# Performance work log

Hardware: AMD Instinct MI355X
Metric: run time of the kernel (lower is better)

## Reference

```python
import jax, jax.numpy as jnp
import numpy as np

N_NODES = 75000
N_EDGES = 1200000


def gcn_conv(x, src, dst, W, b, n):
    # linear transform first (PyG GCNConv applies lin before propagate)
    h = x @ W  # [n, out]
    # add self loops
    loop = jnp.arange(n, dtype=src.dtype)
    s = jnp.concatenate([src, loop])
    d = jnp.concatenate([dst, loop])
    # symmetric normalization: deg computed on destination after self-loops
    deg = jnp.zeros((n,), dtype=h.dtype).at[d].add(1.0)
    dinv = jnp.where(deg > 0, jax.lax.rsqrt(deg), 0.0)
    norm = dinv[s] * dinv[d]  # [E+n]
    msgs = h[s] * norm[:, None]  # gather + scale, [E+n, out]
    out = jax.ops.segment_sum(msgs, d, num_segments=n)  # scatter-add
    return out + b


def setup_inputs() -> dict:
    key = jax.random.key(0)
    ks = jax.random.split(key, 6)
    x = jax.random.normal(ks[0], (N_NODES, 64), dtype=jnp.float32)
    edge_index = jax.random.randint(ks[1], (2, N_EDGES), 0, N_NODES, dtype=jnp.int64)
    # Glorot-ish scaled weights
    W1 = jax.random.normal(ks[2], (64, 64), dtype=jnp.float32) * (1.0 / np.sqrt(64))
    b1 = jax.random.normal(ks[3], (64,), dtype=jnp.float32) * 0.01
    W2 = jax.random.normal(ks[4], (64, 16), dtype=jnp.float32) * (1.0 / np.sqrt(64))
    b2 = jax.random.normal(ks[5], (16,), dtype=jnp.float32) * 0.01
    return {"x": x, "edge_index": edge_index, "W1": W1, "b1": b1, "W2": W2, "b2": b2}


def reference(x, edge_index, W1, b1, W2, b2):
    src, dst = edge_index[0], edge_index[1]
    h = gcn_conv(x, src, dst, W1, b1, N_NODES)
    h = jax.nn.relu(h)
    # dropout is identity in eval mode
    out = gcn_conv(h, src, dst, W2, b2, N_NODES)
    return out
```

## Files before the change

kernel.cpp:

```cpp
#include <hip/hip_runtime.h>


#define NBSHIFT 9
#define BUCKET_NODES 512
#define CAP 10240
#define CHA 8192
#define TA 512
#define TB 512
#define MAXNB 160

__device__ __forceinline__ unsigned bfpack(float a, float b) {
  unsigned ua = __float_as_uint(a), ub = __float_as_uint(b);
  ua += 0x7fffu + ((ua >> 16) & 1u);
  ub += 0x7fffu + ((ub >> 16) & 1u);
  return (ua >> 16) | (ub & 0xffff0000u);
}

__launch_bounds__(TA)
__global__ void kA_bucket(const int* __restrict__ src, const int* __restrict__ dst,
                          int* __restrict__ bucketCur, int* __restrict__ bucketArr,
                          int NB, int E) {
  __shared__ int stage[CHA];
  __shared__ unsigned char binOf[CHA];
  __shared__ int cnt[MAXNB];
  __shared__ int off[MAXNB];
  __shared__ int gpos[MAXNB];
  __shared__ int cursor[MAXNB];
  __shared__ int scanbuf[256];
  int t = threadIdx.x;
  int e0 = blockIdx.x * CHA;

  for (int i = t; i < NB; i += TA) cnt[i] = 0;
  __syncthreads();
  for (int i = t; i < CHA; i += TA) {
    int e = e0 + i;
    if (e < E) atomicAdd(&cnt[dst[e] >> NBSHIFT], 1);
  }
  __syncthreads();
  if (t < 256) scanbuf[t] = (t < NB) ? cnt[t] : 0;
  __syncthreads();
  for (int o = 1; o < 256; o <<= 1) {
    int add = (t < 256 && t >= o) ? scanbuf[t - o] : 0;
    __syncthreads();
    if (t < 256) scanbuf[t] += add;
    __syncthreads();
  }
  if (t < NB) {
    off[t] = scanbuf[t] - cnt[t];
    cursor[t] = off[t];
    gpos[t] = (cnt[t] > 0) ? atomicAdd(&bucketCur[t], cnt[t]) : 0;
  }
  __syncthreads();
  for (int i = t; i < CHA; i += TA) {
    int e = e0 + i;
    if (e < E) {
      int d = dst[e], s = src[e];
      int b = d >> NBSHIFT;
      int p = atomicAdd(&cursor[b], 1);
      stage[p] = (s << NBSHIFT) | (d & (BUCKET_NODES - 1));
      binOf[p] = (unsigned char)b;
    }
  }
  __syncthreads();
  int total = scanbuf[255];
  for (int i = t; i < total; i += TA) {
    int b = binOf[i];
    int destIdx = gpos[b] + (i - off[b]);
    if (destIdx < CAP) bucketArr[b * CAP + destIdx] = stage[i];
  }
}

__global__ void kB_scan(const int* __restrict__ bucketCur, int* __restrict__ bucketBase,
                        int* __restrict__ rp, int NB, int N) {
  __shared__ int s[256];
  int t = threadIdx.x;
  int v = (t < NB) ? min(bucketCur[t], CAP) : 0;
  s[t] = v;
  __syncthreads();
  for (int o = 1; o < 256; o <<= 1) {
    int add = (t >= o) ? s[t - o] : 0;
    __syncthreads();
    s[t] += add;
    __syncthreads();
  }
  if (t < NB) bucketBase[t] = s[t] - v;
  if (t == NB - 1) {
    bucketBase[NB] = s[t];
    rp[N] = s[t];
  }
}

__launch_bounds__(TB)
__global__ void kB_fill(const int* __restrict__ bucketArr, const int* __restrict__ bucketCur,
                        const int* __restrict__ bucketBase,
                        int* __restrict__ rp, float* __restrict__ dinv,
                        int* __restrict__ col, int N) {
  __shared__ int hist[BUCKET_NODES];
  __shared__ int noff[BUCKET_NODES];
  __shared__ int cur[BUCKET_NODES];
  __shared__ int colStage[CAP];
  int b = blockIdx.x;
  int t = threadIdx.x;
  int nE = min(bucketCur[b], CAP);
  int base = b * CAP;

  hist[t] = 0;
  __syncthreads();
  for (int i = t; i < nE; i += TB) {
    atomicAdd(&hist[bucketArr[base + i] & (BUCKET_NODES - 1)], 1);
  }
  __syncthreads();
  int myv = hist[t];
  noff[t] = myv;
  __syncthreads();
  for (int o = 1; o < BUCKET_NODES; o <<= 1) {
    int add = (t >= o) ? noff[t - o] : 0;
    __syncthreads();
    noff[t] += add;
    __syncthreads();
  }
  int excl = noff[t] - myv;
  cur[t] = excl;
  int gnode = b * BUCKET_NODES + t;
  if (gnode < N) {
    rp[gnode] = bucketBase[b] + excl;
    dinv[gnode] = rsqrtf((float)(myv + 1));
  }
  __syncthreads();
  for (int i = t; i < nE; i += TB) {
    int v = bucketArr[base + i];
    int p = atomicAdd(&cur[v & (BUCKET_NODES - 1)], 1);
    colStage[p] = v >> NBSHIFT;
  }
  __syncthreads();
  int gb = bucketBase[b];
  for (int i = t; i < nE; i += TB) col[gb + i] = colStage[i];
}

__launch_bounds__(256)
__global__ void k_gemm64(const float4* __restrict__ X4, const float4* __restrict__ W4,
                         const float* __restrict__ dinv, uint2* __restrict__ outb,
                         int n) {
  __shared__ float4 Xs[64 * 17];
  __shared__ float4 Ws[64 * 16];
  int t = threadIdx.x;
  int base = blockIdx.x * 64;
  {
    int rr = t >> 2, q = t & 3;
    int r = base + rr;
    #pragma unroll
    for (int c = 0; c < 4; c++) {
      float4 v = make_float4(0.f, 0.f, 0.f, 0.f);
      if (r < n) v = X4[r * 16 + q * 4 + c];
      Xs[rr * 17 + q * 4 + c] = v;
      Ws[t + 256 * c] = W4[t + 256 * c];
    }
  }
  __syncthreads();

  int tx = t & 15, ty = t >> 4;
  float4 a0 = make_float4(0.f, 0.f, 0.f, 0.f), a1 = a0, a2 = a0, a3 = a0;
  #pragma unroll
  for (int kb = 0; kb < 16; kb++) {
    float4 x0 = Xs[(ty * 4 + 0) * 17 + kb];
    float4 x1 = Xs[(ty * 4 + 1) * 17 + kb];
    float4 x2 = Xs[(ty * 4 + 2) * 17 + kb];
    float4 x3 = Xs[(ty * 4 + 3) * 17 + kb];
    float4 w0 = Ws[(kb * 4 + 0) * 16 + tx];
    float4 w1 = Ws[(kb * 4 + 1) * 16 + tx];
    float4 w2 = Ws[(kb * 4 + 2) * 16 + tx];
    float4 w3 = Ws[(kb * 4 + 3) * 16 + tx];
    #define FMA4(A, XS) \
      A.x = fmaf(XS.x, w0.x, A.x); A.y = fmaf(XS.x, w0.y, A.y); \
      A.z = fmaf(XS.x, w0.z, A.z); A.w = fmaf(XS.x, w0.w, A.w); \
      A.x = fmaf(XS.y, w1.x, A.x); A.y = fmaf(XS.y, w1.y, A.y); \
      A.z = fmaf(XS.y, w1.z, A.z); A.w = fmaf(XS.y, w1.w, A.w); \
      A.x = fmaf(XS.z, w2.x, A.x); A.y = fmaf(XS.z, w2.y, A.y); \
      A.z = fmaf(XS.z, w2.z, A.z); A.w = fmaf(XS.z, w2.w, A.w); \
      A.x = fmaf(XS.w, w3.x, A.x); A.y = fmaf(XS.w, w3.y, A.y); \
      A.z = fmaf(XS.w, w3.z, A.z); A.w = fmaf(XS.w, w3.w, A.w);
    FMA4(a0, x0) FMA4(a1, x1) FMA4(a2, x2) FMA4(a3, x3)
    #undef FMA4
  }
  #pragma unroll
  for (int i = 0; i < 4; i++) {
    int r = base + ty * 4 + i;
    if (r < n) {
      float s = dinv[r];
      float4 a = (i == 0) ? a0 : (i == 1) ? a1 : (i == 2) ? a2 : a3;
      uint2 pk;
      pk.x = bfpack(a.x * s, a.y * s);
      pk.y = bfpack(a.z * s, a.w * s);
      outb[r * 16 + tx] = pk;
    }
  }
}

__launch_bounds__(256)
__global__ void k_agg64_w2(const uint2* __restrict__ hsb,
                           const int* __restrict__ rp,
                           const int* __restrict__ col,
                           const float* __restrict__ dinv,
                           const float* __restrict__ b1,
                           const float* __restrict__ W2,
                           unsigned* __restrict__ hs2b,
                           int n) {
  int lane = threadIdx.x & 63;
  int c = lane & 15;
  int sub = lane >> 4;
  int node = (blockIdx.x * blockDim.x + threadIdx.x) >> 6;
  if (node >= n) return;

  float4 b14 = ((const float4*)b1)[c];
  float w2r[16];
  #pragma unroll
  for (int i = 0; i < 16; i++) w2r[i] = W2[(sub * 16 + i) * 16 + c];

  int s0 = rp[node], s1 = rp[node + 1];
  int dt = s1 - s0 + 1;
  float ax = 0.f, ay = 0.f, az = 0.f, aw = 0.f;
  int t = sub;
  int i0 = 0, i1 = 0, i2 = 0, i3 = 0;
  if (t < dt)      i0 = (t == 0) ? node : col[s0 + t - 1];
  if (t + 4 < dt)  i1 = col[s0 + t + 3];
  if (t + 8 < dt)  i2 = col[s0 + t + 7];
  if (t + 12 < dt) i3 = col[s0 + t + 11];
  while (t < dt) {
    int c0 = i0, c1 = i1, c2 = i2, c3 = i3;
    bool h1 = (t + 4) < dt, h2 = (t + 8) < dt, h3 = (t + 12) < dt;
    int tn = t + 16;
    if (tn < dt)      i0 = col[s0 + tn - 1];
    if (tn + 4 < dt)  i1 = col[s0 + tn + 3];
    if (tn + 8 < dt)  i2 = col[s0 + tn + 7];
    if (tn + 12 < dt) i3 = col[s0 + tn + 11];
    uint2 u0 = hsb[c0 * 16 + c];
    uint2 u1 = h1 ? hsb[c1 * 16 + c] : make_uint2(0u, 0u);
    uint2 u2 = h2 ? hsb[c2 * 16 + c] : make_uint2(0u, 0u);
    uint2 u3 = h3 ? hsb[c3 * 16 + c] : make_uint2(0u, 0u);
    ax += __uint_as_float(u0.x << 16) + __uint_as_float(u1.x << 16)
        + __uint_as_float(u2.x << 16) + __uint_as_float(u3.x << 16);
    ay += __uint_as_float(u0.x & 0xffff0000u) + __uint_as_float(u1.x & 0xffff0000u)
        + __uint_as_float(u2.x & 0xffff0000u) + __uint_as_float(u3.x & 0xffff0000u);
    az += __uint_as_float(u0.y << 16) + __uint_as_float(u1.y << 16)
        + __uint_as_float(u2.y << 16) + __uint_as_float(u3.y << 16);
    aw += __uint_as_float(u0.y & 0xffff0000u) + __uint_as_float(u1.y & 0xffff0000u)
        + __uint_as_float(u2.y & 0xffff0000u) + __uint_as_float(u3.y & 0xffff0000u);
    t = tn;
  }
  #pragma unroll
  for (int m = 16; m <= 32; m <<= 1) {
    ax += __shfl_xor(ax, m);
    ay += __shfl_xor(ay, m);
    az += __shfl_xor(az, m);
    aw += __shfl_xor(aw, m);
  }
  float dv = dinv[node];
  float hx = fmaxf(ax * dv + b14.x, 0.f);
  float hy = fmaxf(ay * dv + b14.y, 0.f);
  float hz = fmaxf(az * dv + b14.z, 0.f);
  float hw = fmaxf(aw * dv + b14.w, 0.f);

  float part = 0.f;
  #pragma unroll
  for (int i = 0; i < 16; i++) {
    int srcLane = 4 * sub + (i >> 2);
    float h;
    if ((i & 3) == 0)      h = __shfl(hx, srcLane);
    else if ((i & 3) == 1) h = __shfl(hy, srcLane);
    else if ((i & 3) == 2) h = __shfl(hz, srcLane);
    else                   h = __shfl(hw, srcLane);
    part = fmaf(h, w2r[i], part);
  }
  #pragma unroll
  for (int m = 16; m <= 32; m <<= 1) part += __shfl_xor(part, m);
  part *= dv;
  float pnext = __shfl_down(part, 1);
  if (sub == 0 && (c & 1) == 0) {
    hs2b[node * 8 + (c >> 1)] = bfpack(part, pnext);
  }
}

__launch_bounds__(256)
__global__ void k_agg16(const uint2* __restrict__ hs2b,
                        const int* __restrict__ rp,
                        const int* __restrict__ col,
                        const float* __restrict__ dinv,
                        const float* __restrict__ b2,
                        float4* __restrict__ out4,
                        int n) {
  int lane = threadIdx.x & 63;
  int c = lane & 3;
  int sub = lane >> 2;
  int node = (blockIdx.x * blockDim.x + threadIdx.x) >> 6;
  if (node >= n) return;

  int s0 = rp[node], s1 = rp[node + 1];
  int dt = s1 - s0 + 1;
  float ax = 0.f, ay = 0.f, az = 0.f, aw = 0.f;
  int t = sub;
  int i0 = 0, i1 = 0;
  if (t < dt)      i0 = (t == 0) ? node : col[s0 + t - 1];
  if (t + 16 < dt) i1 = col[s0 + t + 15];
  while (t < dt) {
    int c0 = i0, c1 = i1;
    bool h1 = (t + 16) < dt;
    int tn = t + 32;
    if (tn < dt)      i0 = col[s0 + tn - 1];
    if (tn + 16 < dt) i1 = col[s0 + tn + 15];
    uint2 u0 = hs2b[c0 * 4 + c];
    uint2 u1 = h1 ? hs2b[c1 * 4 + c] : make_uint2(0u, 0u);
    ax += __uint_as_float(u0.x << 16) + __uint_as_float(u1.x << 16);
    ay += __uint_as_float(u0.x & 0xffff0000u) + __uint_as_float(u1.x & 0xffff0000u);
    az += __uint_as_float(u0.y << 16) + __uint_as_float(u1.y << 16);
    aw += __uint_as_float(u0.y & 0xffff0000u) + __uint_as_float(u1.y & 0xffff0000u);
    t = tn;
  }
  #pragma unroll
  for (int m = 4; m <= 32; m <<= 1) {
    ax += __shfl_xor(ax, m);
    ay += __shfl_xor(ay, m);
    az += __shfl_xor(az, m);
    aw += __shfl_xor(aw, m);
  }
  if (sub == 0) {
    float dv = dinv[node];
    float4 b24 = ((const float4*)b2)[c];
    float4 o;
    o.x = ax * dv + b24.x;
    o.y = ay * dv + b24.y;
    o.z = az * dv + b24.z;
    o.w = aw * dv + b24.w;
    out4[node * 4 + c] = o;
  }
}

extern "C" void kernel_launch(void* const* d_in, const int* in_sizes, int n_in,
                              void* d_out, int out_size, void* d_ws, size_t ws_size,
                              hipStream_t stream) {
  const float* x  = (const float*)d_in[0];
  const int* edges = (const int*)d_in[1];
  const float* W1 = (const float*)d_in[2];
  const float* b1 = (const float*)d_in[3];
  const float* W2 = (const float*)d_in[4];
  const float* b2 = (const float*)d_in[5];
  float* out = (float*)d_out;

  const int N = in_sizes[0] / 64;
  const int E = in_sizes[1] / 2;
  const int* src = edges;
  const int* dst = edges + E;
  const int NB = (N + BUCKET_NODES - 1) >> NBSHIFT;

  auto align = [](size_t v) { return (v + 255) & ~(size_t)255; };
  char* p = (char*)d_ws;
  float* dinv       = (float*)p; p += align((size_t)N * 4);
  int*   rp         = (int*)p;   p += align((size_t)(N + 1) * 4);
  int*   bucketCur  = (int*)p;   p += align((size_t)MAXNB * 4);
  int*   bucketBase = (int*)p;   p += align((size_t)(MAXNB + 1) * 4);
  int*   col        = (int*)p;   p += align((size_t)E * 4);
  float* hs1        = (float*)p; p += align((size_t)N * 64 * 4);
  float* hs2        = (float*)p; p += align((size_t)N * 16 * 4);
  int* bucketArr = (int*)hs1;

  const int nbA = (E + CHA - 1) / CHA;
  const int nbWave = ((size_t)N * 64 + 255) / 256;

  hipMemsetAsync(bucketCur, 0, (size_t)MAXNB * 4, stream);
  kA_bucket<<<nbA, TA, 0, stream>>>(src, dst, bucketCur, bucketArr, NB, E);
  kB_scan  <<<1, 256, 0, stream>>>(bucketCur, bucketBase, rp, NB, N);
  kB_fill  <<<NB, TB, 0, stream>>>(bucketArr, bucketCur, bucketBase, rp, dinv, col, N);

  k_gemm64  <<<(N + 63) / 64, 256, 0, stream>>>((const float4*)x, (const float4*)W1,
                                                dinv, (uint2*)hs1, N);
  k_agg64_w2<<<nbWave, 256, 0, stream>>>((const uint2*)hs1, rp, col, dinv,
                                         b1, W2, (unsigned*)hs2, N);
  k_agg16   <<<nbWave, 256, 0, stream>>>((const uint2*)hs2, rp, col, dinv,
                                         b2, (float4*)out, N);
}
```

Measured before the change: 129.8 us.

## Fold bucket scan into fill kernel, use wave-shuffle scan, cache dst in registers

Removes the separate single-block kB_scan launch: each kB_fill block computes its own bucket base by summing the preceding bucket counts in shared memory. The per-node prefix scan is replaced by a 64-lane shuffle scan plus a small cross-wave offset, which cuts the number of block-wide barriers. Column indices are scattered directly to global memory instead of being staged through shared memory. kA_bucket keeps dst values in registers so the second pass does not reload them. The trade-offs are a serial loop of up to about 150 iterations on thread 0 of each block and uncoalesced global stores for col.

After: 128.7 us. No clear change (-0.8%).

```diff
diff --git a/kernel.cpp b/kernel.cpp
--- a/kernel.cpp
+++ b/kernel.cpp
@@ -8,6 +8,7 @@
 #define TA 512
 #define TB 512
 #define MAXNB 160
+#define EPT 16
 
 __device__ __forceinline__ unsigned bfpack(float a, float b) {
   unsigned ua = __float_as_uint(a), ub = __float_as_uint(b);
@@ -32,9 +33,12 @@
 
   for (int i = t; i < NB; i += TA) cnt[i] = 0;
   __syncthreads();
-  for (int i = t; i < CHA; i += TA) {
-    int e = e0 + i;
-    if (e < E) atomicAdd(&cnt[dst[e] >> NBSHIFT], 1);
+  int dreg[EPT];
+  #pragma unroll
+  for (int j = 0; j < EPT; j++) {
+    int e = e0 + t + j * TA;
+    dreg[j] = (e < E) ? dst[e] : -1;
+    if (dreg[j] >= 0) atomicAdd(&cnt[dreg[j] >> NBSHIFT], 1);
   }
   __syncthreads();
   if (t < 256) scanbuf[t] = (t < NB) ? cnt[t] : 0;
@@ -51,10 +55,11 @@
     gpos[t] = (cnt[t] > 0) ? atomicAdd(&bucketCur[t], cnt[t]) : 0;
   }
   __syncthreads();
-  for (int i = t; i < CHA; i += TA) {
-    int e = e0 + i;
-    if (e < E) {
-      int d = dst[e], s = src[e];
+  #pragma unroll
+  for (int j = 0; j < EPT; j++) {
+    int e = e0 + t + j * TA;
+    if (dreg[j] >= 0) {
+      int d = dreg[j], s = src[e];
       int b = d >> NBSHIFT;
       int p = atomicAdd(&cursor[b], 1);
       stage[p] = (s << NBSHIFT) | (d & (BUCKET_NODES - 1));
@@ -70,71 +75,59 @@
   }
 }
 
-__global__ void kB_scan(const int* __restrict__ bucketCur, int* __restrict__ bucketBase,
-                        int* __restrict__ rp, int NB, int N) {
-  __shared__ int s[256];
-  int t = threadIdx.x;
-  int v = (t < NB) ? min(bucketCur[t], CAP) : 0;
-  s[t] = v;
-  __syncthreads();
-  for (int o = 1; o < 256; o <<= 1) {
-    int add = (t >= o) ? s[t - o] : 0;
-    __syncthreads();
-    s[t] += add;
-    __syncthreads();
-  }
-  if (t < NB) bucketBase[t] = s[t] - v;
-  if (t == NB - 1) {
-    bucketBase[NB] = s[t];
-    rp[N] = s[t];
-  }
-}
-
 __launch_bounds__(TB)
 __global__ void kB_fill(const int* __restrict__ bucketArr, const int* __restrict__ bucketCur,
-                        const int* __restrict__ bucketBase,
                         int* __restrict__ rp, float* __restrict__ dinv,
-                        int* __restrict__ col, int N) {
+                        int* __restrict__ col, int N, int NB) {
+  __shared__ int cnts[MAXNB];
   __shared__ int hist[BUCKET_NODES];
-  __shared__ int noff[BUCKET_NODES];
   __shared__ int cur[BUCKET_NODES];
-  __shared__ int colStage[CAP];
+  __shared__ int wsum[8], woff[8];
+  __shared__ int s_base;
   int b = blockIdx.x;
   int t = threadIdx.x;
   int nE = min(bucketCur[b], CAP);
   int base = b * CAP;
 
+  if (t < NB) cnts[t] = min(bucketCur[t], CAP);
   hist[t] = 0;
   __syncthreads();
-  for (int i = t; i < nE; i += TB) {
+  for (int i = t; i < nE; i += TB)
     atomicAdd(&hist[bucketArr[base + i] & (BUCKET_NODES - 1)], 1);
-  }
   __syncthreads();
   int myv = hist[t];
-  noff[t] = myv;
-  __syncthreads();
-  for (int o = 1; o < BUCKET_NODES; o <<= 1) {
-    int add = (t >= o) ? noff[t - o] : 0;
-    __syncthreads();
-    noff[t] += add;
-    __syncthreads();
-  }
-  int excl = noff[t] - myv;
-  cur[t] = excl;
+  int lane = t & 63, w = t >> 6;
+  int incl = myv;
+  #pragma unroll
+  for (int o = 1; o < 64; o <<= 1) {
+    int v = __shfl_up(incl, o);
+    if (lane >= o) incl += v;
+  }
+  if (lane == 63) wsum[w] = incl;
+  __syncthreads();
+  if (t == 0) {
+    int acc = 0;
+    for (int i = 0; i < b; i++) acc += cnts[i];
+    s_base = acc;
+    int a2 = 0;
+    #pragma unroll
+    for (int i = 0; i < 8; i++) { woff[i] = a2; a2 += wsum[i]; }
+    if (b == NB - 1) rp[N] = acc + nE;
+  }
+  __syncthreads();
+  int gexcl = s_base + woff[w] + (incl - myv);
+  cur[t] = gexcl;
   int gnode = b * BUCKET_NODES + t;
   if (gnode < N) {
-    rp[gnode] = bucketBase[b] + excl;
+    rp[gnode] = gexcl;
     dinv[gnode] = rsqrtf((float)(myv + 1));
   }
   __syncthreads();
   for (int i = t; i < nE; i += TB) {
     int v = bucketArr[base + i];
     int p = atomicAdd(&cur[v & (BUCKET_NODES - 1)], 1);
-    colStage[p] = v >> NBSHIFT;
-  }
-  __syncthreads();
-  int gb = bucketBase[b];
-  for (int i = t; i < nE; i += TB) col[gb + i] = colStage[i];
+    col[p] = v >> NBSHIFT;
+  }
 }
 
 __launch_bounds__(256)
@@ -356,7 +349,6 @@
   float* dinv       = (float*)p; p += align((size_t)N * 4);
   int*   rp         = (int*)p;   p += align((size_t)(N + 1) * 4);
   int*   bucketCur  = (int*)p;   p += align((size_t)MAXNB * 4);
-  int*   bucketBase = (int*)p;   p += align((size_t)(MAXNB + 1) * 4);
   int*   col        = (int*)p;   p += align((size_t)E * 4);
   float* hs1        = (float*)p; p += align((size_t)N * 64 * 4);
   float* hs2        = (float*)p; p += align((size_t)N * 16 * 4);
@@ -367,8 +359,7 @@
 
   hipMemsetAsync(bucketCur, 0, (size_t)MAXNB * 4, stream);
   kA_bucket<<<nbA, TA, 0, stream>>>(src, dst, bucketCur, bucketArr, NB, E);
-  kB_scan  <<<1, 256, 0, stream>>>(bucketCur, bucketBase, rp, NB, N);
-  kB_fill  <<<NB, TB, 0, stream>>>(bucketArr, bucketCur, bucketBase, rp, dinv, col, N);
+  kB_fill  <<<NB, TB, 0, stream>>>(bucketArr, bucketCur, rp, dinv, col, N, NB);
 
   k_gemm64  <<<(N + 63) / 64, 256, 0, stream>>>((const float4*)x, (const float4*)W1,
                                                 dinv, (uint2*)hs1, N);
```
